# Optimization experiments

Hardware: AMD Instinct MI355X
Metric: run time of the kernel (lower is better)

Reference implementation:

```python
import jax, jax.numpy as jnp
import numpy as np

B, S, H, W = 16, 512, 768, 8


def _enumerate_spans(S, W):
    # same enumeration order as the torch triple loop: for i, for j in [i, min(i+W, S)-1]
    starts, widths = [], []
    for i in range(S):
        for w in range(1, min(W, S - i) + 1):
            starts.append(i)
            widths.append(w)
    return np.asarray(starts, np.int32), np.asarray(widths, np.int32)


def setup_inputs() -> dict:
    key = jax.random.key(0)
    k1, k2, k3 = jax.random.split(key, 3)
    embeddings = jax.random.normal(k1, (B, S, H), dtype=jnp.float32)
    w_lin = jax.random.normal(k2, (2 * H + 1, H), dtype=jnp.float32) * 0.02
    b_lin = jax.random.normal(k3, (H,), dtype=jnp.float32) * 0.02
    starts, widths = _enumerate_spans(S, W)
    return {
        "embeddings": embeddings,
        "w_lin": w_lin,
        "b_lin": b_lin,
        "span_starts": jnp.asarray(starts),
        "span_widths": jnp.asarray(widths),
    }


def reference(embeddings, w_lin, b_lin, span_starts, span_widths):
    Bb, Ss, Hh = embeddings.shape
    cls_emb = embeddings[:, 0, :]  # [B, H]

    # Sliding-window running max: pooled[k, b, i, :] = max(embeddings[b, i:i+k+1, :])
    neg = jnp.full((Bb, W - 1, Hh), -jnp.inf, embeddings.dtype)
    padded = jnp.concatenate([embeddings, neg], axis=1)  # [B, S+W-1, H]
    cm = embeddings
    pools = [cm]
    for k in range(1, W):
        cm = jnp.maximum(cm, padded[:, k:k + Ss, :])
        pools.append(cm)
    pooled = jnp.stack(pools, axis=0)  # [W, B, S, H]

    # Gather each span's max-pooled embedding: [N, B, H] -> [B, N, H]
    span_max = pooled[span_widths - 1, :, span_starts, :]
    span_max = jnp.transpose(span_max, (1, 0, 2))

    N = span_starts.shape[0]
    cls_b = jnp.broadcast_to(cls_emb[:, None, :], (Bb, N, Hh))
    width_f = jnp.broadcast_to(
        span_widths.astype(embeddings.dtype)[None, :, None], (Bb, N, 1))
    feats = jnp.concatenate([span_max, cls_b, width_f], axis=-1)  # [B, N, 2H+1]

    span_reps = jnp.einsum("bnf,fh->bnh", feats, w_lin) + b_lin
    token_inputs = cls_emb  # [B, H]
    return token_inputs, span_reps.reshape(Bb * N, Hh)
```

## Files before the change

kernel.cpp:

```cpp
#include <hip/hip_runtime.h>
#include <hip/hip_bf16.h>
#include <stdint.h>

typedef float  f32x4  __attribute__((ext_vector_type(4)));
typedef __bf16 bf16x8 __attribute__((ext_vector_type(8)));
typedef __bf16 bf16x4 __attribute__((ext_vector_type(4)));
typedef short  s16x8  __attribute__((ext_vector_type(8)));

static constexpr int Bc = 16, Sc = 512, Hc = 768, NSPAN = 4068;
static constexpr int BM = 256, BN = 256, BK = 64, KS = Hc / BK;

__global__ __launch_bounds__(256)
void prep_w1t(const float* __restrict__ w_lin, unsigned short* __restrict__ w1t) {
  __shared__ __align__(16) unsigned short T[64][80];
  int bidk = blockIdx.x % 12, bidn = blockIdx.x / 12;
  int k0 = bidk * 64, n0 = bidn * 64;
  int tid = threadIdx.x;
#pragma unroll
  for (int p = 0; p < 16; ++p) {
    int idx = p * 256 + tid;
    int kl = idx >> 6, nl = idx & 63;
    float v = w_lin[(size_t)(k0 + kl) * Hc + (n0 + nl)];
    __bf16 bv = (__bf16)v;
    T[nl][kl] = __builtin_bit_cast(unsigned short, bv);
  }
  __syncthreads();
#pragma unroll
  for (int qq = 0; qq < 2; ++qq) {
    int q = qq * 256 + tid;
    int nl = q >> 3, c = q & 7;
    int n = n0 + nl;
    s16x8 v = *(const s16x8*)(&T[nl][c * 8]);
    *(s16x8*)(w1t + (size_t)n * Hc + k0 + c * 8) = v;
  }
}

__global__ __launch_bounds__(256)
void cls_proj_kernel(const float* __restrict__ emb, const float* __restrict__ w_lin,
                     const float* __restrict__ b_lin, float* __restrict__ out,
                     float* __restrict__ cls_proj) {
  __shared__ float cls_s[Hc];
  int b = blockIdx.x / 3, hc = blockIdx.x % 3;
  int tid = threadIdx.x;
  const float* cls = emb + (size_t)b * Sc * Hc;
  for (int i = tid; i < Hc; i += 256) cls_s[i] = cls[i];
  __syncthreads();
  int h = hc * 256 + tid;
  const float* wp = w_lin + (size_t)Hc * Hc + h;
  float p0 = 0, p1 = 0, p2 = 0, p3 = 0, p4 = 0, p5 = 0, p6 = 0, p7 = 0;
  for (int f = 0; f < Hc; f += 8) {
    p0 += cls_s[f + 0] * wp[(size_t)(f + 0) * Hc];
    p1 += cls_s[f + 1] * wp[(size_t)(f + 1) * Hc];
    p2 += cls_s[f + 2] * wp[(size_t)(f + 2) * Hc];
    p3 += cls_s[f + 3] * wp[(size_t)(f + 3) * Hc];
    p4 += cls_s[f + 4] * wp[(size_t)(f + 4) * Hc];
    p5 += cls_s[f + 5] * wp[(size_t)(f + 5) * Hc];
    p6 += cls_s[f + 6] * wp[(size_t)(f + 6) * Hc];
    p7 += cls_s[f + 7] * wp[(size_t)(f + 7) * Hc];
  }
  float acc = b_lin[h] + (((p0 + p1) + (p2 + p3)) + ((p4 + p5) + (p6 + p7)));
  cls_proj[b * Hc + h] = acc;
  out[b * Hc + h] = cls_s[h];
}

__global__ __launch_bounds__(512, 2)
void span_gemm(const float* __restrict__ emb, const unsigned short* __restrict__ w1t,
               const float* __restrict__ cls_proj, const float* __restrict__ w_lin,
               float* __restrict__ out) {
  __shared__ __align__(16) unsigned short Ald[2][BM * BK];

  int wg = blockIdx.x;
  int wgid = (wg & 7) * 96 + (wg >> 3);
  int tile_n = wgid % 3, tile_m = wgid / 3;
  int b = tile_m >> 4;
  int s0 = (tile_m & 15) << 5;
  int n0 = tile_n << 8;
  int tid = threadIdx.x;
  int wid = tid >> 6, lane = tid & 63;
  int wave_m = wid >> 2, wave_n = wid & 3;
  int lq = lane >> 4, lr = lane & 15;

  const char* embC = (const char*)(emb + (size_t)b * Sc * Hc);

  int bi = tid >> 4, bkq = tid & 15;
  uint32_t rowoff[8];
#pragma unroll
  for (int t = 0; t < 8; ++t) {
    int r = s0 + bi + t;
    if (r > 511) r = 511;
    rowoff[t] = (uint32_t)r * (Hc * 4) + bkq * 16;
  }
  int awbase = (bi << 10) + ((bkq & 1) << 3);

  const unsigned short* bb = w1t + (size_t)(n0 + (wave_n << 6) + lr) * Hc + (lq << 3);

  f32x4 acc[8][4];
  f32x4 zer = {0.f, 0.f, 0.f, 0.f};
#pragma unroll
  for (int i = 0; i < 8; ++i)
#pragma unroll
    for (int j = 0; j < 4; ++j) acc[i][j] = zer;

  f32x4 rv[8];
  f32x4 cm;
  bf16x8 bfrA[4], bfrB[4];

#define SCHED0 __builtin_amdgcn_sched_barrier(0)

#define LOAD_RV(koff)                                                          \
  _Pragma("unroll") for (int t = 0; t < 8; ++t)                                \
      rv[t] = *(const f32x4*)(embC + rowoff[t] + (koff));

#define LOAD_BFR(dst, koff)                                                    \
  _Pragma("unroll") for (int ni = 0; ni < 4; ++ni)                             \
      dst[ni] = *(const bf16x8*)(const void*)(bb + (size_t)ni * 16 * Hc + (koff));

#define BUILD_T(an, t)                                                         \
  {                                                                            \
    if ((t) == 0) cm = rv[0];                                                  \
    else {                                                                     \
      cm[0] = fmaxf(cm[0], rv[t][0]); cm[1] = fmaxf(cm[1], rv[t][1]);          \
      cm[2] = fmaxf(cm[2], rv[t][2]); cm[3] = fmaxf(cm[3], rv[t][3]);          \
    }                                                                          \
    bf16x4 p;                                                                  \
    p[0] = (__bf16)cm[0]; p[1] = (__bf16)cm[1];                                \
    p[2] = (__bf16)cm[2]; p[3] = (__bf16)cm[3];                                \
    int off = awbase + ((t) << 7) + (((bkq >> 1) ^ (t)) << 4);                 \
    *(uint2*)((an) + off) = __builtin_bit_cast(uint2, p);                      \
  }

#define QUAD(ab, mh, kk, bfr)                                                  \
  {                                                                            \
    bf16x8 af[4];                                                              \
    int cf = ((kk) << 2) + lq;                                                 \
    _Pragma("unroll") for (int mi = 0; mi < 4; ++mi) {                         \
      int m = (wave_m << 7) + ((((mh) << 2) + mi) << 4) + lr;                  \
      af[mi] = *(const bf16x8*)((ab) + (m << 7) + ((cf ^ (m & 7)) << 4));      \
    }                                                                          \
    __builtin_amdgcn_s_setprio(1);                                             \
    _Pragma("unroll") for (int mi = 0; mi < 4; ++mi)                           \
      _Pragma("unroll") for (int ni = 0; ni < 4; ++ni)                         \
        acc[((mh) << 2) + mi][ni] = __builtin_amdgcn_mfma_f32_16x16x32_bf16(   \
            af[mi], bfr[ni], acc[((mh) << 2) + mi][ni], 0, 0, 0);              \
    __builtin_amdgcn_s_setprio(0);                                             \
  }

  LOAD_RV(0);
  {
    char* an0 = (char*)Ald[0];
#pragma unroll
    for (int t = 0; t < 8; ++t) BUILD_T(an0, t);
  }
  LOAD_BFR(bfrA, 0);
  LOAD_RV(256);
  asm volatile("s_waitcnt lgkmcnt(0)" ::: "memory");
  SCHED0;
  __builtin_amdgcn_s_barrier();
  SCHED0;

  for (int kt = 0; kt < KS; ++kt) {
    int cur = kt & 1, nb = cur ^ 1;
    const char* ab = (const char*)Ald[cur];
    char* an = (char*)Ald[nb];

    LOAD_BFR(bfrB, kt * 64 + 32);
    QUAD(ab, 0, 0, bfrA);
    SCHED0;
    QUAD(ab, 1, 0, bfrA);
    SCHED0;
    if (kt + 1 < KS) {
      LOAD_BFR(bfrA, (kt + 1) * 64);
#pragma unroll
      for (int t = 0; t < 4; ++t) BUILD_T(an, t);
    }
    QUAD(ab, 0, 1, bfrB);
    SCHED0;
    if (kt + 1 < KS) {
#pragma unroll
      for (int t = 4; t < 8; ++t) BUILD_T(an, t);
    }
    if (kt + 2 < KS) LOAD_RV((kt + 2) * 256);
    QUAD(ab, 1, 1, bfrB);
    if (kt + 1 < KS) {
      asm volatile("s_waitcnt lgkmcnt(0)" ::: "memory");
      SCHED0;
      __builtin_amdgcn_s_barrier();
      SCHED0;
    }
  }

  const float* w2p = w_lin + (size_t)(2 * Hc) * Hc;
  float* outp = out + Bc * Hc;
  int swb = (tile_m & 15) << 8;
  float cp[4], w2[4];
#pragma unroll
  for (int ni = 0; ni < 4; ++ni) {
    int h = n0 + (wave_n << 6) + (ni << 4) + lr;
    cp[ni] = cls_proj[b * Hc + h];
    w2[ni] = w2p[h];
  }
  int hbase = n0 + (wave_n << 6) + lr;
#pragma unroll
  for (int mi = 0; mi < 8; ++mi) {
#pragma unroll
    for (int j = 0; j < 4; ++j) {
      int m = (wave_m << 7) + (mi << 4) + (lq << 2) + j;
      int sw = swb + m;
      int s = sw >> 3, w = (sw & 7) + 1;
      if (s + w <= 512) {
        int nsp = (s <= 504) ? sw
                             : (NSPAN - (((512 - s) * (513 - s)) >> 1) + w - 1);
        float* rowp = outp + ((size_t)b * NSPAN + nsp) * Hc + hbase;
        float wf = (float)w;
#pragma unroll
        for (int ni = 0; ni < 4; ++ni)
          rowp[ni << 4] = acc[mi][ni][j] + cp[ni] + wf * w2[ni];
      }
    }
  }
}

extern "C" void kernel_launch(void* const* d_in, const int* in_sizes, int n_in,
                              void* d_out, int out_size, void* d_ws, size_t ws_size,
                              hipStream_t stream) {
  const float* emb = (const float*)d_in[0];
  const float* w_lin = (const float*)d_in[1];
  const float* b_lin = (const float*)d_in[2];
  unsigned short* w1t = (unsigned short*)d_ws;
  float* cls_proj = (float*)((char*)d_ws + (size_t)Hc * Hc * 2);
  float* out = (float*)d_out;

  hipLaunchKernelGGL(prep_w1t, dim3(144), dim3(256), 0, stream, w_lin, w1t);
  hipLaunchKernelGGL(cls_proj_kernel, dim3(48), dim3(256), 0, stream, emb, w_lin, b_lin, out, cls_proj);
  hipLaunchKernelGGL(span_gemm, dim3(768), dim3(512), 0, stream, emb, w1t, cls_proj, w_lin, out);
}
```

Measured before the change: 136.6 us.

## Materialize pooled A operand in workspace and run a four-stage async-LDS GEMM pipeline

Adds a build_a kernel that writes the running-max pooled spans as swizzled bf16 rows into a ~100MB workspace. The GEMM then streams A and B tiles straight into LDS with global_load_lds across a four-deep buffer ring, instead of computing the max pooling inside the GEMM loop. prep_w1t gains an option to write B in the matching swizzle. The aim is to drop the VALU pooling and register-staging work from the MFMA loop. The cost is an extra ~100MB write and read of HBM traffic. A fallback keeps the old fused kernel when the workspace is too small, so it is unclear which path runs by default.

```diff
diff --git a/kernel.cpp b/kernel.cpp
--- a/kernel.cpp
+++ b/kernel.cpp
@@ -1,6 +1,9 @@
 #include <hip/hip_runtime.h>
 #include <hip/hip_bf16.h>
 #include <stdint.h>
+
+#define AS1 __attribute__((address_space(1)))
+#define AS3 __attribute__((address_space(3)))
 
 typedef float  f32x4  __attribute__((ext_vector_type(4)));
 typedef __bf16 bf16x8 __attribute__((ext_vector_type(8)));
@@ -8,10 +11,9 @@
 typedef short  s16x8  __attribute__((ext_vector_type(8)));
 
 static constexpr int Bc = 16, Sc = 512, Hc = 768, NSPAN = 4068;
-static constexpr int BM = 256, BN = 256, BK = 64, KS = Hc / BK;
 
 __global__ __launch_bounds__(256)
-void prep_w1t(const float* __restrict__ w_lin, unsigned short* __restrict__ w1t) {
+void prep_w1t(const float* __restrict__ w_lin, unsigned short* __restrict__ w1t, int swz) {
   __shared__ __align__(16) unsigned short T[64][80];
   int bidk = blockIdx.x % 12, bidn = blockIdx.x / 12;
   int k0 = bidk * 64, n0 = bidn * 64;
@@ -28,10 +30,17 @@
 #pragma unroll
   for (int qq = 0; qq < 2; ++qq) {
     int q = qq * 256 + tid;
-    int nl = q >> 3, c = q & 7;
+    int nl = q >> 3, cc = q & 7;
     int n = n0 + nl;
-    s16x8 v = *(const s16x8*)(&T[nl][c * 8]);
-    *(s16x8*)(w1t + (size_t)n * Hc + k0 + c * 8) = v;
+    s16x8 v = *(const s16x8*)(&T[nl][cc * 8]);
+    size_t off;
+    if (swz) {
+      int q8 = (k0 >> 3) + cc;
+      off = (size_t)n * 1536 + (size_t)(q8 >> 2) * 64 + (size_t)((q8 & 3) ^ (n & 3)) * 16;
+    } else {
+      off = (size_t)n * 1536 + (size_t)k0 * 2 + (size_t)cc * 16;
+    }
+    *(s16x8*)((char*)w1t + off) = v;
   }
 }
 
@@ -63,12 +72,192 @@
   out[b * Hc + h] = cls_s[h];
 }
 
-__global__ __launch_bounds__(512, 2)
-void span_gemm(const float* __restrict__ emb, const unsigned short* __restrict__ w1t,
+__global__ __launch_bounds__(256)
+void build_a(const float* __restrict__ emb, unsigned short* __restrict__ a_ws) {
+  int blk = blockIdx.x;
+  int b = blk >> 6, sb = blk & 63;
+  int tid = threadIdx.x;
+  int si = tid >> 5, kc = tid & 31;
+  int s = (sb << 3) + si;
+  const char* embB = (const char*)(emb + (size_t)b * Sc * Hc);
+  uint32_t roff[8];
+#pragma unroll
+  for (int t = 0; t < 8; ++t) {
+    int r = s + t;
+    if (r > 511) r = 511;
+    roff[t] = (uint32_t)r * (Hc * 4);
+  }
+  char* obase = (char*)a_ws + (size_t)((b * 512 + s) * 8) * 1536;
+#pragma unroll
+  for (int j = 0; j < 3; ++j) {
+    int q8 = kc + (j << 5);
+    uint32_t srcoff = (uint32_t)q8 * 32;
+    f32x4 c0, c1;
+#pragma unroll
+    for (int t = 0; t < 8; ++t) {
+      f32x4 a0 = *(const f32x4*)(embB + roff[t] + srcoff);
+      f32x4 a1 = *(const f32x4*)(embB + roff[t] + srcoff + 16);
+      if (t == 0) { c0 = a0; c1 = a1; }
+      else {
+        c0[0] = fmaxf(c0[0], a0[0]); c0[1] = fmaxf(c0[1], a0[1]);
+        c0[2] = fmaxf(c0[2], a0[2]); c0[3] = fmaxf(c0[3], a0[3]);
+        c1[0] = fmaxf(c1[0], a1[0]); c1[1] = fmaxf(c1[1], a1[1]);
+        c1[2] = fmaxf(c1[2], a1[2]); c1[3] = fmaxf(c1[3], a1[3]);
+      }
+      bf16x8 p;
+      p[0] = (__bf16)c0[0]; p[1] = (__bf16)c0[1]; p[2] = (__bf16)c0[2]; p[3] = (__bf16)c0[3];
+      p[4] = (__bf16)c1[0]; p[5] = (__bf16)c1[1]; p[6] = (__bf16)c1[2]; p[7] = (__bf16)c1[3];
+      size_t doff = (size_t)t * 1536 + (size_t)(q8 >> 2) * 64 + (size_t)((q8 & 3) ^ (t & 3)) * 16;
+      *(bf16x8*)(obase + doff) = p;
+    }
+  }
+}
+
+__global__ __launch_bounds__(512, 1)
+void gemm_pipe(const unsigned short* __restrict__ a_ws, const unsigned short* __restrict__ w1t,
                const float* __restrict__ cls_proj, const float* __restrict__ w_lin,
                float* __restrict__ out) {
-  __shared__ __align__(16) unsigned short Ald[2][BM * BK];
-
+  extern __shared__ __align__(16) char ldsb[];
+
+  int wg = blockIdx.x;
+  int wgid = (wg & 7) * 96 + (wg >> 3);
+  int tile_n = wgid % 3, tile_m = wgid / 3;
+  int b = tile_m >> 4;
+  int n0 = tile_n << 8;
+  int tid = threadIdx.x;
+  int wid = tid >> 6, lane = tid & 63;
+  int wave_m = wid >> 2, wave_n = wid & 3;
+  int lq = lane >> 4, lr = lane & 15;
+
+  const char* aw = (const char*)a_ws + ((size_t)tile_m << 8) * 1536;
+  const char* bw = (const char*)w1t + (size_t)n0 * 1536;
+  int srow = tid >> 2, schunk = tid & 3;
+
+  const float* w2p = w_lin + (size_t)(2 * Hc) * Hc;
+  float cp[4], w2[4];
+#pragma unroll
+  for (int ni = 0; ni < 4; ++ni) {
+    int h = n0 + (wave_n << 6) + (ni << 4) + lr;
+    cp[ni] = cls_proj[b * Hc + h];
+    w2[ni] = w2p[h];
+  }
+
+  f32x4 acc[8][4];
+  f32x4 zer = {0.f, 0.f, 0.f, 0.f};
+#pragma unroll
+  for (int i = 0; i < 8; ++i)
+#pragma unroll
+    for (int j = 0; j < 4; ++j) acc[i][j] = zer;
+
+  bf16x8 bfr[4];
+
+#define SB __builtin_amdgcn_sched_barrier(0)
+
+#define STAGE_A(kt) {                                                          \
+    const char* s_ = aw + (size_t)srow * 1536 + (size_t)(kt) * 64 + (schunk << 4); \
+    char* d_ = ldsb + (((kt) & 3) << 15) + (tid << 4);                         \
+    __builtin_amdgcn_global_load_lds((const AS1 uint32_t*)s_, (AS3 uint32_t*)d_, 16, 0, 0); \
+    __builtin_amdgcn_global_load_lds((const AS1 uint32_t*)(s_ + 128 * 1536), (AS3 uint32_t*)(d_ + 8192), 16, 0, 0); }
+
+#define STAGE_B(kt) {                                                          \
+    const char* s_ = bw + (size_t)srow * 1536 + (size_t)(kt) * 64 + (schunk << 4); \
+    char* d_ = ldsb + (((kt) & 3) << 15) + 16384 + (tid << 4);                 \
+    __builtin_amdgcn_global_load_lds((const AS1 uint32_t*)s_, (AS3 uint32_t*)d_, 16, 0, 0); \
+    __builtin_amdgcn_global_load_lds((const AS1 uint32_t*)(s_ + 128 * 1536), (AS3 uint32_t*)(d_ + 8192), 16, 0, 0); }
+
+#define PH0(kt, DOSTAGE) {                                                     \
+    const char* Ab_ = ldsb + (((kt) & 3) << 15);                               \
+    const char* Bb_ = Ab_ + 16384;                                             \
+    _Pragma("unroll") for (int ni = 0; ni < 4; ++ni) {                         \
+      int n = (wave_n << 6) + (ni << 4) + lr;                                  \
+      bfr[ni] = *(const bf16x8*)(Bb_ + n * 64 + ((lq ^ (n & 3)) << 4));        \
+    }                                                                          \
+    bf16x8 af[4];                                                              \
+    _Pragma("unroll") for (int mi = 0; mi < 4; ++mi) {                         \
+      int m = (wave_m << 7) + (mi << 4) + lr;                                  \
+      af[mi] = *(const bf16x8*)(Ab_ + m * 64 + ((lq ^ (m & 3)) << 4));         \
+    }                                                                          \
+    if (DOSTAGE) { STAGE_A((kt) + 3); }                                        \
+    SB; __builtin_amdgcn_s_barrier(); SB;                                      \
+    __builtin_amdgcn_s_setprio(1);                                             \
+    _Pragma("unroll") for (int mi = 0; mi < 4; ++mi)                           \
+      _Pragma("unroll") for (int ni = 0; ni < 4; ++ni)                         \
+        acc[mi][ni] = __builtin_amdgcn_mfma_f32_16x16x32_bf16(af[mi], bfr[ni], acc[mi][ni], 0, 0, 0); \
+    __builtin_amdgcn_s_setprio(0);                                             \
+    __builtin_amdgcn_s_barrier(); }
+
+#define PH1(kt, DOSTAGE, WAITASM) {                                            \
+    const char* Ab_ = ldsb + (((kt) & 3) << 15);                               \
+    bf16x8 af[4];                                                              \
+    _Pragma("unroll") for (int mi = 0; mi < 4; ++mi) {                         \
+      int m = (wave_m << 7) + 64 + (mi << 4) + lr;                             \
+      af[mi] = *(const bf16x8*)(Ab_ + m * 64 + ((lq ^ (m & 3)) << 4));         \
+    }                                                                          \
+    if (DOSTAGE) { STAGE_B((kt) + 3); }                                        \
+    SB; __builtin_amdgcn_s_barrier(); SB;                                      \
+    __builtin_amdgcn_s_setprio(1);                                             \
+    _Pragma("unroll") for (int mi = 0; mi < 4; ++mi)                           \
+      _Pragma("unroll") for (int ni = 0; ni < 4; ++ni)                         \
+        acc[4 + mi][ni] = __builtin_amdgcn_mfma_f32_16x16x32_bf16(af[mi], bfr[ni], acc[4 + mi][ni], 0, 0, 0); \
+    __builtin_amdgcn_s_setprio(0);                                             \
+    SB; asm volatile(WAITASM ::: "memory"); SB;                                \
+    __builtin_amdgcn_s_barrier(); }
+
+  STAGE_A(-3 + 3); STAGE_B(0);
+  STAGE_A(1 - 3 + 3);
+  {
+    const char* s_ = aw + (size_t)srow * 1536 + (size_t)1 * 64 + (schunk << 4);
+    char* d_ = ldsb + ((1 & 3) << 15) + (tid << 4);
+    __builtin_amdgcn_global_load_lds((const AS1 uint32_t*)s_, (AS3 uint32_t*)d_, 16, 0, 0);
+    __builtin_amdgcn_global_load_lds((const AS1 uint32_t*)(s_ + 128 * 1536), (AS3 uint32_t*)(d_ + 8192), 16, 0, 0);
+  }
+  STAGE_B(1);
+  {
+    const char* s_ = aw + (size_t)srow * 1536 + (size_t)2 * 64 + (schunk << 4);
+    char* d_ = ldsb + ((2 & 3) << 15) + (tid << 4);
+    __builtin_amdgcn_global_load_lds((const AS1 uint32_t*)s_, (AS3 uint32_t*)d_, 16, 0, 0);
+    __builtin_amdgcn_global_load_lds((const AS1 uint32_t*)(s_ + 128 * 1536), (AS3 uint32_t*)(d_ + 8192), 16, 0, 0);
+  }
+  STAGE_B(2);
+  SB; asm volatile("s_waitcnt vmcnt(8)" ::: "memory"); SB;
+  __builtin_amdgcn_s_barrier(); SB;
+
+  for (int kt = 0; kt < 21; ++kt) {
+    PH0(kt, 1);
+    PH1(kt, 1, "s_waitcnt vmcnt(8)");
+  }
+  PH0(21, 0); PH1(21, 0, "s_waitcnt vmcnt(4)");
+  PH0(22, 0); PH1(22, 0, "s_waitcnt vmcnt(0)");
+  PH0(23, 0); PH1(23, 0, "s_nop 0");
+
+  float* outp = out + Bc * Hc;
+  int swb = (tile_m & 15) << 8;
+  int hbase = n0 + (wave_n << 6) + lr;
+#pragma unroll
+  for (int mi = 0; mi < 8; ++mi) {
+#pragma unroll
+    for (int j = 0; j < 4; ++j) {
+      int m = (wave_m << 7) + (mi << 4) + (lq << 2) + j;
+      int sw = swb + m;
+      int s = sw >> 3, w = (sw & 7) + 1;
+      if (s + w <= 512) {
+        int nsp = (s <= 504) ? sw
+                             : (NSPAN - (((512 - s) * (513 - s)) >> 1) + w - 1);
+        float* rowp = outp + ((size_t)b * NSPAN + nsp) * Hc + hbase;
+        float wf = (float)w;
+#pragma unroll
+        for (int ni = 0; ni < 4; ++ni)
+          rowp[ni << 4] = acc[mi][ni][j] + cp[ni] + wf * w2[ni];
+      }
+    }
+  }
+}
+
+__global__ __launch_bounds__(512, 2)
+void span_gemm_fused(const float* __restrict__ emb, const unsigned short* __restrict__ w1t,
+                     const float* __restrict__ cls_proj, const float* __restrict__ w_lin,
+                     float* __restrict__ out) {
+  __shared__ __align__(16) unsigned short Ald[2][256 * 64];
   int wg = blockIdx.x;
   int wgid = (wg & 7) * 96 + (wg >> 3);
   int tile_n = wgid % 3, tile_m = wgid / 3;
@@ -79,9 +268,7 @@
   int wid = tid >> 6, lane = tid & 63;
   int wave_m = wid >> 2, wave_n = wid & 3;
   int lq = lane >> 4, lr = lane & 15;
-
   const char* embC = (const char*)(emb + (size_t)b * Sc * Hc);
-
   int bi = tid >> 4, bkq = tid & 15;
   uint32_t rowoff[8];
 #pragma unroll
@@ -91,104 +278,74 @@
     rowoff[t] = (uint32_t)r * (Hc * 4) + bkq * 16;
   }
   int awbase = (bi << 10) + ((bkq & 1) << 3);
-
   const unsigned short* bb = w1t + (size_t)(n0 + (wave_n << 6) + lr) * Hc + (lq << 3);
-
   f32x4 acc[8][4];
   f32x4 zer = {0.f, 0.f, 0.f, 0.f};
 #pragma unroll
   for (int i = 0; i < 8; ++i)
 #pragma unroll
     for (int j = 0; j < 4; ++j) acc[i][j] = zer;
-
   f32x4 rv[8];
   f32x4 cm;
   bf16x8 bfrA[4], bfrB[4];
-
-#define SCHED0 __builtin_amdgcn_sched_barrier(0)
-
-#define LOAD_RV(koff)                                                          \
-  _Pragma("unroll") for (int t = 0; t < 8; ++t)                                \
-      rv[t] = *(const f32x4*)(embC + rowoff[t] + (koff));
-
-#define LOAD_BFR(dst, koff)                                                    \
-  _Pragma("unroll") for (int ni = 0; ni < 4; ++ni)                             \
-      dst[ni] = *(const bf16x8*)(const void*)(bb + (size_t)ni * 16 * Hc + (koff));
-
-#define BUILD_T(an, t)                                                         \
-  {                                                                            \
-    if ((t) == 0) cm = rv[0];                                                  \
-    else {                                                                     \
-      cm[0] = fmaxf(cm[0], rv[t][0]); cm[1] = fmaxf(cm[1], rv[t][1]);          \
-      cm[2] = fmaxf(cm[2], rv[t][2]); cm[3] = fmaxf(cm[3], rv[t][3]);          \
-    }                                                                          \
-    bf16x4 p;                                                                  \
-    p[0] = (__bf16)cm[0]; p[1] = (__bf16)cm[1];                                \
-    p[2] = (__bf16)cm[2]; p[3] = (__bf16)cm[3];                                \
-    int off = awbase + ((t) << 7) + (((bkq >> 1) ^ (t)) << 4);                 \
-    *(uint2*)((an) + off) = __builtin_bit_cast(uint2, p);                      \
-  }
-
-#define QUAD(ab, mh, kk, bfr)                                                  \
-  {                                                                            \
-    bf16x8 af[4];                                                              \
-    int cf = ((kk) << 2) + lq;                                                 \
-    _Pragma("unroll") for (int mi = 0; mi < 4; ++mi) {                         \
-      int m = (wave_m << 7) + ((((mh) << 2) + mi) << 4) + lr;                  \
-      af[mi] = *(const bf16x8*)((ab) + (m << 7) + ((cf ^ (m & 7)) << 4));      \
-    }                                                                          \
-    __builtin_amdgcn_s_setprio(1);                                             \
-    _Pragma("unroll") for (int mi = 0; mi < 4; ++mi)                           \
-      _Pragma("unroll") for (int ni = 0; ni < 4; ++ni)                         \
-        acc[((mh) << 2) + mi][ni] = __builtin_amdgcn_mfma_f32_16x16x32_bf16(   \
-            af[mi], bfr[ni], acc[((mh) << 2) + mi][ni], 0, 0, 0);              \
-    __builtin_amdgcn_s_setprio(0);                                             \
-  }
-
-  LOAD_RV(0);
+#define FLOAD_RV(koff) _Pragma("unroll") for (int t = 0; t < 8; ++t) rv[t] = *(const f32x4*)(embC + rowoff[t] + (koff));
+#define FLOAD_BFR(dst, koff) _Pragma("unroll") for (int ni = 0; ni < 4; ++ni) dst[ni] = *(const bf16x8*)(const void*)(bb + (size_t)ni * 16 * Hc + (koff));
+#define FBUILD_T(an, t) { \
+    if ((t) == 0) cm = rv[0]; \
+    else { cm[0] = fmaxf(cm[0], rv[t][0]); cm[1] = fmaxf(cm[1], rv[t][1]); cm[2] = fmaxf(cm[2], rv[t][2]); cm[3] = fmaxf(cm[3], rv[t][3]); } \
+    bf16x4 p; p[0] = (__bf16)cm[0]; p[1] = (__bf16)cm[1]; p[2] = (__bf16)cm[2]; p[3] = (__bf16)cm[3]; \
+    int off = awbase + ((t) << 7) + (((bkq >> 1) ^ (t)) << 4); \
+    *(uint2*)((an) + off) = __builtin_bit_cast(uint2, p); }
+#define FQUAD(ab, mh, kk, bfr) { \
+    bf16x8 af[4]; int cf = ((kk) << 2) + lq; \
+    _Pragma("unroll") for (int mi = 0; mi < 4; ++mi) { \
+      int m = (wave_m << 7) + ((((mh) << 2) + mi) << 4) + lr; \
+      af[mi] = *(const bf16x8*)((ab) + (m << 7) + ((cf ^ (m & 7)) << 4)); } \
+    __builtin_amdgcn_s_setprio(1); \
+    _Pragma("unroll") for (int mi = 0; mi < 4; ++mi) \
+      _Pragma("unroll") for (int ni = 0; ni < 4; ++ni) \
+        acc[((mh) << 2) + mi][ni] = __builtin_amdgcn_mfma_f32_16x16x32_bf16(af[mi], bfr[ni], acc[((mh) << 2) + mi][ni], 0, 0, 0); \
+    __builtin_amdgcn_s_setprio(0); }
+  FLOAD_RV(0);
   {
     char* an0 = (char*)Ald[0];
 #pragma unroll
-    for (int t = 0; t < 8; ++t) BUILD_T(an0, t);
-  }
-  LOAD_BFR(bfrA, 0);
-  LOAD_RV(256);
+    for (int t = 0; t < 8; ++t) FBUILD_T(an0, t);
+  }
+  FLOAD_BFR(bfrA, 0);
+  FLOAD_RV(256);
   asm volatile("s_waitcnt lgkmcnt(0)" ::: "memory");
-  SCHED0;
+  __builtin_amdgcn_sched_barrier(0);
   __builtin_amdgcn_s_barrier();
-  SCHED0;
-
-  for (int kt = 0; kt < KS; ++kt) {
+  for (int kt = 0; kt < 12; ++kt) {
     int cur = kt & 1, nb = cur ^ 1;
     const char* ab = (const char*)Ald[cur];
     char* an = (char*)Ald[nb];
-
-    LOAD_BFR(bfrB, kt * 64 + 32);
-    QUAD(ab, 0, 0, bfrA);
-    SCHED0;
-    QUAD(ab, 1, 0, bfrA);
-    SCHED0;
-    if (kt + 1 < KS) {
-      LOAD_BFR(bfrA, (kt + 1) * 64);
-#pragma unroll
-      for (int t = 0; t < 4; ++t) BUILD_T(an, t);
-    }
-    QUAD(ab, 0, 1, bfrB);
-    SCHED0;
-    if (kt + 1 < KS) {
-#pragma unroll
-      for (int t = 4; t < 8; ++t) BUILD_T(an, t);
-    }
-    if (kt + 2 < KS) LOAD_RV((kt + 2) * 256);
-    QUAD(ab, 1, 1, bfrB);
-    if (kt + 1 < KS) {
+    FLOAD_BFR(bfrB, kt * 64 + 32);
+    FQUAD(ab, 0, 0, bfrA);
+    __builtin_amdgcn_sched_barrier(0);
+    FQUAD(ab, 1, 0, bfrA);
+    __builtin_amdgcn_sched_barrier(0);
+    if (kt + 1 < 12) {
+      FLOAD_BFR(bfrA, (kt + 1) * 64);
+#pragma unroll
+      for (int t = 0; t < 4; ++t) FBUILD_T(an, t);
+    }
+    FQUAD(ab, 0, 1, bfrB);
+    __builtin_amdgcn_sched_barrier(0);
+    if (kt + 1 < 12) {
+#pragma unroll
+      for (int t = 4; t < 8; ++t) FBUILD_T(an, t);
+    }
+    if (kt + 2 < 12) FLOAD_RV((kt + 2) * 256);
+    FQUAD(ab, 1, 1, bfrB);
+    if (kt + 1 < 12) {
       asm volatile("s_waitcnt lgkmcnt(0)" ::: "memory");
-      SCHED0;
+      __builtin_amdgcn_sched_barrier(0);
       __builtin_amdgcn_s_barrier();
-      SCHED0;
-    }
-  }
-
+      __builtin_amdgcn_sched_barrier(0);
+    }
+  }
   const float* w2p = w_lin + (size_t)(2 * Hc) * Hc;
   float* outp = out + Bc * Hc;
   int swb = (tile_m & 15) << 8;
@@ -208,8 +365,7 @@
       int sw = swb + m;
       int s = sw >> 3, w = (sw & 7) + 1;
       if (s + w <= 512) {
-        int nsp = (s <= 504) ? sw
-                             : (NSPAN - (((512 - s) * (513 - s)) >> 1) + w - 1);
+        int nsp = (s <= 504) ? sw : (NSPAN - (((512 - s) * (513 - s)) >> 1) + w - 1);
         float* rowp = outp + ((size_t)b * NSPAN + nsp) * Hc + hbase;
         float wf = (float)w;
 #pragma unroll
@@ -227,10 +383,24 @@
   const float* w_lin = (const float*)d_in[1];
   const float* b_lin = (const float*)d_in[2];
   unsigned short* w1t = (unsigned short*)d_ws;
-  float* cls_proj = (float*)((char*)d_ws + (size_t)Hc * Hc * 2);
+  float* cls_proj = (float*)((char*)d_ws + 1179648);
+  unsigned short* a_ws = (unsigned short*)((char*)d_ws + 1228800);
   float* out = (float*)d_out;
 
-  hipLaunchKernelGGL(prep_w1t, dim3(144), dim3(256), 0, stream, w_lin, w1t);
-  hipLaunchKernelGGL(cls_proj_kernel, dim3(48), dim3(256), 0, stream, emb, w_lin, b_lin, out, cls_proj);
-  hipLaunchKernelGGL(span_gemm, dim3(768), dim3(512), 0, stream, emb, w1t, cls_proj, w_lin, out);
-}
+  size_t need = 1228800ull + 100663296ull;
+  if (ws_size >= need) {
+    hipLaunchKernelGGL(prep_w1t, dim3(144), dim3(256), 0, stream, w_lin, w1t, 1);
+    hipLaunchKernelGGL(cls_proj_kernel, dim3(48), dim3(256), 0, stream, emb, w_lin, b_lin, out, cls_proj);
+    hipLaunchKernelGGL(build_a, dim3(1024), dim3(256), 0, stream, emb, a_ws);
+    static int attr_set = 0;
+    if (!attr_set) {
+      hipFuncSetAttribute((const void*)gemm_pipe, hipFuncAttributeMaxDynamicSharedMemorySize, 131072);
+      attr_set = 1;
+    }
+    hipLaunchKernelGGL(gemm_pipe, dim3(768), dim3(512), 131072, stream, a_ws, w1t, cls_proj, w_lin, out);
+  } else {
+    hipLaunchKernelGGL(prep_w1t, dim3(144), dim3(256), 0, stream, w_lin, w1t, 0);
+    hipLaunchKernelGGL(cls_proj_kernel, dim3(48), dim3(256), 0, stream, emb, w_lin, b_lin, out, cls_proj);
+    hipLaunchKernelGGL(span_gemm_fused, dim3(768), dim3(512), 0, stream, emb, w1t, cls_proj, w_lin, out);
+  }
+}
```

Result: slower. 153.8 us (+12.6%).
